# Performance work log

Measured on AMD Instinct MI355X. Metric: run time of the kernel, lower is better.

The kernel has to match this reference:

```python
import jax, jax.numpy as jnp
import numpy as np

N_NODES = 100000
N_EDGES = 1600000
IN_F, HID, N_CLS = 128, 128, 2


def setup_inputs() -> dict:
    key = jax.random.key(0)
    ks = jax.random.split(key, 6)
    return {
        "in_feat": jax.random.normal(ks[0], (N_NODES, IN_F), dtype=jnp.float32),
        "W1": jax.random.normal(ks[1], (IN_F, HID), dtype=jnp.float32) * 0.05,
        "b1": jnp.zeros((HID,), dtype=jnp.float32),
        "W2": jax.random.normal(ks[2], (HID, N_CLS), dtype=jnp.float32) * 0.05,
        "b2": jnp.zeros((N_CLS,), dtype=jnp.float32),
        "src": jax.random.randint(ks[3], (N_EDGES,), 0, N_NODES, dtype=jnp.int32),
        "dst": jax.random.randint(ks[4], (N_EDGES,), 0, N_NODES, dtype=jnp.int32),
    }


def reference(in_feat, W1, b1, W2, b2, src, dst):
    N = in_feat.shape[0]
    ones = jnp.ones(src.shape[0], dtype=in_feat.dtype)
    deg_out = jax.ops.segment_sum(ones, src, num_segments=N)
    deg_in = jax.ops.segment_sum(ones, dst, num_segments=N)
    # DGL norm='both' with allow_zero_in_degree: inf -> 0 for zero-degree nodes
    ninv_out = jnp.where(deg_out > 0, deg_out ** -0.5, 0.0)[:, None]
    ninv_in = jnp.where(deg_in > 0, deg_in ** -0.5, 0.0)[:, None]

    def gconv(x, W, b):
        h = x * ninv_out
        if W.shape[0] > W.shape[1]:
            # mult W first (DGL optimization when in_feats > out_feats)
            h = h @ W
            h = jax.ops.segment_sum(h[src], dst, num_segments=N)
        else:
            h = jax.ops.segment_sum(h[src], dst, num_segments=N)
            h = h @ W
        return h * ninv_in + b

    h = jax.nn.relu(gconv(in_feat, W1, b1))
    return gconv(h, W2, b2)
```

## Files before the change

kernel.cpp:

```cpp
#include <hip/hip_runtime.h>

#define IN_F 128
#define HID  128
#define NB_SHIFT 8
#define NBKT 512
#define NCHUNK 256

typedef __bf16 bf16x8 __attribute__((ext_vector_type(8)));
typedef float f32x4 __attribute__((ext_vector_type(4)));
union U8 { uint4 u; bf16x8 v; };

__device__ __forceinline__ unsigned int bfround(float x) {
    unsigned int u = __float_as_uint(x);
    return (u + 0x7fffu + ((u >> 16) & 1u)) >> 16;
}
__device__ __forceinline__ unsigned int pack2(float a, float b) {
    return bfround(a) | (bfround(b) << 16);
}
__device__ __forceinline__ float lo_f(unsigned int u) { return __uint_as_float(u << 16); }
__device__ __forceinline__ float hi_f(unsigned int u) { return __uint_as_float(u & 0xffff0000u); }

__global__ __launch_bounds__(256)
void countAB_kernel(const int* __restrict__ src, const int* __restrict__ dst,
                    int* __restrict__ cd, int* __restrict__ cs, int E, int epc) {
    __shared__ int hd[NBKT], hs[NBKT];
    int tid = threadIdx.x, c = blockIdx.x;
    hd[tid] = 0; hd[tid + 256] = 0; hs[tid] = 0; hs[tid + 256] = 0;
    __syncthreads();
    int lo = c * epc, hi = min(lo + epc, E);
    for (int i = lo + tid; i < hi; i += 256) {
        atomicAdd(&hd[dst[i] >> NB_SHIFT], 1);
        atomicAdd(&hs[src[i] >> NB_SHIFT], 1);
    }
    __syncthreads();
    cd[c * NBKT + tid] = hd[tid]; cd[c * NBKT + tid + 256] = hd[tid + 256];
    cs[c * NBKT + tid] = hs[tid]; cs[c * NBKT + tid + 256] = hs[tid + 256];
}

__global__ __launch_bounds__(256)
void scanB1_kernel(int* __restrict__ cd, int* __restrict__ cs,
                   int* __restrict__ btd, int* __restrict__ bts) {
    __shared__ int sd[256];
    int b = blockIdx.x, tid = threadIdx.x;
    int* arr = (b < NBKT) ? cd : cs;
    int* bt  = (b < NBKT) ? btd : bts;
    int col = b & (NBKT - 1);
    int v = arr[tid * NBKT + col];
    sd[tid] = v; __syncthreads();
    for (int off = 1; off < 256; off <<= 1) {
        int t = (tid >= off) ? sd[tid - off] : 0;
        __syncthreads();
        sd[tid] += t;
        __syncthreads();
    }
    arr[tid * NBKT + col] = sd[tid] - v;
    if (tid == 255) bt[col] = sd[255];
}

__global__ __launch_bounds__(512)
void scanB2_kernel(const int* __restrict__ btd, const int* __restrict__ bts,
                   int* __restrict__ bbd, int* __restrict__ bbs,
                   int* __restrict__ row_ptr, int N, int E) {
    __shared__ int sd[512];
    int tid = threadIdx.x;
    const int* bt = blockIdx.x ? bts : btd;
    int* bb = blockIdx.x ? bbs : bbd;
    int v = bt[tid];
    sd[tid] = v; __syncthreads();
    for (int off = 1; off < 512; off <<= 1) {
        int t = (tid >= off) ? sd[tid - off] : 0;
        __syncthreads();
        sd[tid] += t;
        __syncthreads();
    }
    bb[tid] = sd[tid] - v;
    if (tid == 511) bb[512] = sd[511];
    if (blockIdx.x == 0 && tid == 0) row_ptr[N] = E;
}

__global__ __launch_bounds__(256)
void scatterAB_kernel(const int* __restrict__ src, const int* __restrict__ dst,
                      const int* __restrict__ cd, const int* __restrict__ cs,
                      const int* __restrict__ bbd, const int* __restrict__ bbs,
                      int* __restrict__ pairs, unsigned char* __restrict__ sbytes,
                      int E, int epc) {
    __shared__ int curd[NBKT], curs[NBKT];
    int tid = threadIdx.x, c = blockIdx.x;
    curd[tid]       = cd[c * NBKT + tid]       + bbd[tid];
    curd[tid + 256] = cd[c * NBKT + tid + 256] + bbd[tid + 256];
    curs[tid]       = cs[c * NBKT + tid]       + bbs[tid];
    curs[tid + 256] = cs[c * NBKT + tid + 256] + bbs[tid + 256];
    __syncthreads();
    int lo = c * epc, hi = min(lo + epc, E);
    for (int i = lo + tid; i < hi; i += 256) {
        int s = src[i], d = dst[i];
        int pd = atomicAdd(&curd[d >> NB_SHIFT], 1);
        pairs[pd] = s | ((d & 255) << 17);
        int ps = atomicAdd(&curs[s >> NB_SHIFT], 1);
        sbytes[ps] = (unsigned char)(s & 255);
    }
}

__global__ __launch_bounds__(256)
void buildD_kernel(const int* __restrict__ pairs, const int* __restrict__ bbd,
                   int* __restrict__ row_ptr, float* __restrict__ ninv_in,
                   int* __restrict__ eidx, int N) {
    __shared__ int cnt[256], sd[256], cursor[256];
    int b = blockIdx.x, tid = threadIdx.x;
    int beg = bbd[b], end = bbd[b + 1];
    cnt[tid] = 0;
    __syncthreads();
    for (int i = beg + tid; i < end; i += 256)
        atomicAdd(&cnt[(pairs[i] >> 17) & 255], 1);
    __syncthreads();
    int v = cnt[tid];
    sd[tid] = v; __syncthreads();
    for (int off = 1; off < 256; off <<= 1) {
        int t = (tid >= off) ? sd[tid - off] : 0;
        __syncthreads();
        sd[tid] += t;
        __syncthreads();
    }
    int excl = sd[tid] - v;
    int node = (b << NB_SHIFT) + tid;
    if (node < N) {
        row_ptr[node] = beg + excl;
        ninv_in[node] = (v > 0) ? rsqrtf((float)v) : 0.0f;
    }
    cursor[tid] = beg + excl;
    __syncthreads();
    for (int i = beg + tid; i < end; i += 256) {
        int p = pairs[i];
        int pos = atomicAdd(&cursor[(p >> 17) & 255], 1);
        eidx[pos] = p & 0x1FFFF;
    }
}

__global__ __launch_bounds__(256)
void buildDsrc_kernel(const unsigned char* __restrict__ sbytes, const int* __restrict__ bbs,
                      float* __restrict__ ninv_out, int N) {
    __shared__ int cnt[256];
    int b = blockIdx.x, tid = threadIdx.x;
    int beg = bbs[b], end = bbs[b + 1];
    cnt[tid] = 0;
    __syncthreads();
    for (int i = beg + tid; i < end; i += 256)
        atomicAdd(&cnt[sbytes[i]], 1);
    __syncthreads();
    int node = (b << NB_SHIFT) + tid;
    if (node < N) {
        int v = cnt[tid];
        ninv_out[node] = (v > 0) ? rsqrtf((float)v) : 0.0f;
    }
}

__global__ __launch_bounds__(256)
void conv_kernel(const float* __restrict__ in_feat, const float* __restrict__ ninv_out,
                 unsigned int* __restrict__ xb, int N) {
    int gid = blockIdx.x * 256 + threadIdx.x;
    if (gid >= N * 32) return;
    int r = gid >> 5, q = gid & 31;
    float no = ninv_out[r];
    float4 v = ((const float4*)in_feat)[(long)r * 32 + q];
    uint2 o;
    o.x = pack2(v.x * no, v.y * no);
    o.y = pack2(v.z * no, v.w * no);
    ((uint2*)xb)[(long)r * 32 + q] = o;
}

__global__ __launch_bounds__(256)
void agg1_kernel(const unsigned int* __restrict__ xb, const int* __restrict__ row_ptr,
                 const int* __restrict__ eidx, unsigned int* __restrict__ Bb, int N) {
    int wave = threadIdx.x >> 6;
    int lane = threadIdx.x & 63;
    int d = blockIdx.x * 4 + wave;
    if (d >= N) return;
    int beg = row_ptr[d], end = row_ptr[d + 1];
    float ax = 0.f, ay = 0.f;
    int j = beg;
    for (; j + 8 <= end; j += 8) {
        int s0 = eidx[j+0], s1 = eidx[j+1], s2 = eidx[j+2], s3 = eidx[j+3];
        int s4 = eidx[j+4], s5 = eidx[j+5], s6 = eidx[j+6], s7 = eidx[j+7];
        unsigned int u0 = xb[(long)s0*64+lane], u1 = xb[(long)s1*64+lane];
        unsigned int u2 = xb[(long)s2*64+lane], u3 = xb[(long)s3*64+lane];
        unsigned int u4 = xb[(long)s4*64+lane], u5 = xb[(long)s5*64+lane];
        unsigned int u6 = xb[(long)s6*64+lane], u7 = xb[(long)s7*64+lane];
        ax += lo_f(u0) + lo_f(u1) + lo_f(u2) + lo_f(u3)
            + lo_f(u4) + lo_f(u5) + lo_f(u6) + lo_f(u7);
        ay += hi_f(u0) + hi_f(u1) + hi_f(u2) + hi_f(u3)
            + hi_f(u4) + hi_f(u5) + hi_f(u6) + hi_f(u7);
    }
    for (; j + 2 <= end; j += 2) {
        unsigned int u0 = xb[(long)eidx[j]*64+lane], u1 = xb[(long)eidx[j+1]*64+lane];
        ax += lo_f(u0) + lo_f(u1);
        ay += hi_f(u0) + hi_f(u1);
    }
    if (j < end) {
        unsigned int u = xb[(long)eidx[j]*64+lane];
        ax += lo_f(u); ay += hi_f(u);
    }
    Bb[(long)d * 64 + lane] = pack2(ax, ay);
}

#define MM_ROWS 64
__global__ __launch_bounds__(256)
void mm1_kernel(const unsigned int* __restrict__ Bb, const float* __restrict__ W1,
                const float* __restrict__ b1, const float* __restrict__ ninv_in,
                const float* __restrict__ ninv_out, const float* __restrict__ W2,
                float* __restrict__ t, int N) {
    __shared__ unsigned int w1t[128 * 68];
    int tid = threadIdx.x;
    int wave = tid >> 6, lane = tid & 63;
    int row0 = blockIdx.x * MM_ROWS;

    {
        int c = tid & 127;
        int kh = tid >> 7;
#pragma unroll 8
        for (int j = 0; j < 32; ++j) {
            int k2 = j * 2 + kh;
            float a = W1[(k2 * 2)     * HID + c];
            float b = W1[(k2 * 2 + 1) * HID + c];
            w1t[c * 68 + k2] = pack2(a, b);
        }
    }

    int m = lane & 15;
    int kg = lane >> 4;
    float  b1r[8];
    float2 w2r[8];
    const float2* W2v = (const float2*)W2;
#pragma unroll
    for (int ct = 0; ct < 8; ++ct) {
        int n = m + 16 * ct;
        b1r[ct] = b1[n];
        w2r[ct] = W2v[n];
    }

    int r = row0 + wave * 16 + m;
    U8 afrag[4];
    if (r < N) {
#pragma unroll
        for (int ks = 0; ks < 4; ++ks)
            afrag[ks].u = *(const uint4*)&Bb[(long)r * 64 + ks * 16 + kg * 4];
    } else {
#pragma unroll
        for (int ks = 0; ks < 4; ++ks)
            afrag[ks].u = make_uint4(0u, 0u, 0u, 0u);
    }
    __syncthreads();

    f32x4 acc[8];
#pragma unroll
    for (int ct = 0; ct < 8; ++ct) acc[ct] = (f32x4){0.f, 0.f, 0.f, 0.f};

#pragma unroll
    for (int ks = 0; ks < 4; ++ks) {
#pragma unroll
        for (int ct = 0; ct < 8; ++ct) {
            U8 bf;
            bf.u = *(const uint4*)&w1t[(m + 16 * ct) * 68 + ks * 16 + kg * 4];
            acc[ct] = __builtin_amdgcn_mfma_f32_16x16x32_bf16(afrag[ks].v, bf.v, acc[ct], 0, 0, 0);
        }
    }

#pragma unroll
    for (int reg = 0; reg < 4; ++reg) {
        int grow = row0 + wave * 16 + kg * 4 + reg;
        int cg = min(grow, N - 1);
        float ni = ninv_in[cg];
        float p0 = 0.f, p1 = 0.f;
#pragma unroll
        for (int ct = 0; ct < 8; ++ct) {
            float h = fmaxf(acc[ct][reg] * ni + b1r[ct], 0.f);
            p0 += h * w2r[ct].x;
            p1 += h * w2r[ct].y;
        }
#pragma unroll
        for (int off = 8; off >= 1; off >>= 1) {
            p0 += __shfl_xor(p0, off, 16);
            p1 += __shfl_xor(p1, off, 16);
        }
        if (m == 0 && grow < N) {
            float no = ninv_out[grow];
            ((float2*)t)[grow] = make_float2(p0 * no, p1 * no);
        }
    }
}

__global__ void final2_kernel(const float* __restrict__ t, const int* __restrict__ row_ptr,
                              const int* __restrict__ eidx, const float* __restrict__ ninv_in,
                              const float* __restrict__ b2, float* __restrict__ out, int N) {
    int i = blockIdx.x * blockDim.x + threadIdx.x;
    if (i >= N) return;
    int beg = row_ptr[i], end = row_ptr[i + 1];
    const float2* t2 = (const float2*)t;
    float ax = 0.f, ay = 0.f;
    int j = beg;
    for (; j + 4 <= end; j += 4) {
        float2 v0 = t2[eidx[j]], v1 = t2[eidx[j+1]], v2 = t2[eidx[j+2]], v3 = t2[eidx[j+3]];
        ax += v0.x + v1.x + v2.x + v3.x;
        ay += v0.y + v1.y + v2.y + v3.y;
    }
    for (; j < end; ++j) {
        float2 v = t2[eidx[j]];
        ax += v.x; ay += v.y;
    }
    float ni = ninv_in[i];
    float2 o;
    o.x = ax * ni + b2[0];
    o.y = ay * ni + b2[1];
    ((float2*)out)[i] = o;
}

extern "C" void kernel_launch(void* const* d_in, const int* in_sizes, int n_in,
                              void* d_out, int out_size, void* d_ws, size_t ws_size,
                              hipStream_t stream) {
    const float* in_feat = (const float*)d_in[0];
    const float* W1      = (const float*)d_in[1];
    const float* b1      = (const float*)d_in[2];
    const float* W2      = (const float*)d_in[3];
    const float* b2      = (const float*)d_in[4];
    const int*   src     = (const int*)d_in[5];
    const int*   dst     = (const int*)d_in[6];
    int N = in_sizes[0] / IN_F;
    int E = in_sizes[5];
    int NB = (N + 255) >> 8;

    unsigned int* Bb  = (unsigned int*)d_ws;
    int*   pairs      = (int*)Bb;
    unsigned char* sbytes = (unsigned char*)(Bb + E);
    unsigned int* xb  = Bb + (size_t)64 * N;
    float* ninv_out   = (float*)(xb + (size_t)64 * N);
    float* ninv_in    = ninv_out + N;
    float* t          = ninv_in + N;
    int*   row_ptr    = (int*)(t + (size_t)2 * N);
    int*   eidx       = row_ptr + N + 1;
    int*   cd         = eidx + E;
    int*   cs         = cd + NCHUNK * NBKT;
    int*   btd        = cs + NCHUNK * NBKT;
    int*   bts        = btd + NBKT;
    int*   bbd        = bts + NBKT;
    int*   bbs        = bbd + NBKT + 1;

    int epc = (E + NCHUNK - 1) / NCHUNK;

    countAB_kernel<<<NCHUNK, 256, 0, stream>>>(src, dst, cd, cs, E, epc);
    scanB1_kernel<<<2 * NBKT, 256, 0, stream>>>(cd, cs, btd, bts);
    scanB2_kernel<<<2, 512, 0, stream>>>(btd, bts, bbd, bbs, row_ptr, N, E);
    scatterAB_kernel<<<NCHUNK, 256, 0, stream>>>(src, dst, cd, cs, bbd, bbs,
                                                 pairs, sbytes, E, epc);
    buildD_kernel<<<NB, 256, 0, stream>>>(pairs, bbd, row_ptr, ninv_in, eidx, N);
    buildDsrc_kernel<<<NB, 256, 0, stream>>>(sbytes, bbs, ninv_out, N);

    conv_kernel<<<(N * 32 + 255) / 256, 256, 0, stream>>>(in_feat, ninv_out, xb, N);

    agg1_kernel<<<(N + 3) / 4, 256, 0, stream>>>(xb, row_ptr, eidx, Bb, N);

    mm1_kernel<<<(N + MM_ROWS - 1) / MM_ROWS, 256, 0, stream>>>(
        Bb, W1, b1, ninv_in, ninv_out, W2, t, N);

    final2_kernel<<<(N + 255) / 256, 256, 0, stream>>>(
        t, row_ptr, eidx, ninv_in, b2, (float*)d_out, N);
}
```

Measured before the change: 258.6 us.

## Merge degree kernels, pretranspose W1 once, widen agg1 gathers to 8-byte loads

Folds the source-degree normalization kernel into the destination CSR build kernel as extra blocks, removing one launch. Packs W1 into bf16 pairs once, using extra blocks of the scan kernel, so each mm1 block loads the packed tile with vector copies instead of strided fp32 loads. agg1 now gives each half-wave a different edge and has lanes fetch uint2 (four bf16 values), combining the halves with a cross-half shuffle. This issues fewer, wider gather loads, at the cost of idle half-waves on nodes with odd degree and a shuffle reduction.

Result: no change. 257.2 us (-0.5%).

```diff
diff --git a/kernel.cpp b/kernel.cpp
--- a/kernel.cpp
+++ b/kernel.cpp
@@ -60,9 +60,18 @@
 __global__ __launch_bounds__(512)
 void scanB2_kernel(const int* __restrict__ btd, const int* __restrict__ bts,
                    int* __restrict__ bbd, int* __restrict__ bbs,
-                   int* __restrict__ row_ptr, int N, int E) {
+                   int* __restrict__ row_ptr, const float* __restrict__ W1,
+                   unsigned int* __restrict__ w1tb, int N, int E) {
+    int tid = threadIdx.x;
+    if (blockIdx.x >= 2) {
+        int idx = (blockIdx.x - 2) * 512 + tid;
+        int c = idx & 127, k2 = idx >> 7;
+        float a = W1[(2 * k2)     * HID + c];
+        float b = W1[(2 * k2 + 1) * HID + c];
+        w1tb[c * 64 + k2] = pack2(a, b);
+        return;
+    }
     __shared__ int sd[512];
-    int tid = threadIdx.x;
     const int* bt = blockIdx.x ? bts : btd;
     int* bb = blockIdx.x ? bbs : bbd;
     int v = bt[tid];
@@ -102,11 +111,29 @@
 }
 
 __global__ __launch_bounds__(256)
-void buildD_kernel(const int* __restrict__ pairs, const int* __restrict__ bbd,
-                   int* __restrict__ row_ptr, float* __restrict__ ninv_in,
-                   int* __restrict__ eidx, int N) {
+void buildD2_kernel(const int* __restrict__ pairs, const unsigned char* __restrict__ sbytes,
+                    const int* __restrict__ bbd, const int* __restrict__ bbs,
+                    int* __restrict__ row_ptr, float* __restrict__ ninv_in,
+                    float* __restrict__ ninv_out, int* __restrict__ eidx,
+                    int N, int NB) {
     __shared__ int cnt[256], sd[256], cursor[256];
-    int b = blockIdx.x, tid = threadIdx.x;
+    int tid = threadIdx.x;
+    if (blockIdx.x >= NB) {
+        int b = blockIdx.x - NB;
+        int beg = bbs[b], end = bbs[b + 1];
+        cnt[tid] = 0;
+        __syncthreads();
+        for (int i = beg + tid; i < end; i += 256)
+            atomicAdd(&cnt[sbytes[i]], 1);
+        __syncthreads();
+        int node = (b << NB_SHIFT) + tid;
+        if (node < N) {
+            int v = cnt[tid];
+            ninv_out[node] = (v > 0) ? rsqrtf((float)v) : 0.0f;
+        }
+        return;
+    }
+    int b = blockIdx.x;
     int beg = bbd[b], end = bbd[b + 1];
     cnt[tid] = 0;
     __syncthreads();
@@ -133,24 +160,6 @@
         int p = pairs[i];
         int pos = atomicAdd(&cursor[(p >> 17) & 255], 1);
         eidx[pos] = p & 0x1FFFF;
-    }
-}
-
-__global__ __launch_bounds__(256)
-void buildDsrc_kernel(const unsigned char* __restrict__ sbytes, const int* __restrict__ bbs,
-                      float* __restrict__ ninv_out, int N) {
-    __shared__ int cnt[256];
-    int b = blockIdx.x, tid = threadIdx.x;
-    int beg = bbs[b], end = bbs[b + 1];
-    cnt[tid] = 0;
-    __syncthreads();
-    for (int i = beg + tid; i < end; i += 256)
-        atomicAdd(&cnt[sbytes[i]], 1);
-    __syncthreads();
-    int node = (b << NB_SHIFT) + tid;
-    if (node < N) {
-        int v = cnt[tid];
-        ninv_out[node] = (v > 0) ? rsqrtf((float)v) : 0.0f;
     }
 }
 
@@ -173,38 +182,55 @@
                  const int* __restrict__ eidx, unsigned int* __restrict__ Bb, int N) {
     int wave = threadIdx.x >> 6;
     int lane = threadIdx.x & 63;
+    int half = lane >> 5;
+    int hl   = lane & 31;
     int d = blockIdx.x * 4 + wave;
     if (d >= N) return;
     int beg = row_ptr[d], end = row_ptr[d + 1];
-    float ax = 0.f, ay = 0.f;
+    const uint2* x2 = (const uint2*)xb;
+    float ax = 0.f, ay = 0.f, az = 0.f, aw = 0.f;
     int j = beg;
-    for (; j + 8 <= end; j += 8) {
-        int s0 = eidx[j+0], s1 = eidx[j+1], s2 = eidx[j+2], s3 = eidx[j+3];
-        int s4 = eidx[j+4], s5 = eidx[j+5], s6 = eidx[j+6], s7 = eidx[j+7];
-        unsigned int u0 = xb[(long)s0*64+lane], u1 = xb[(long)s1*64+lane];
-        unsigned int u2 = xb[(long)s2*64+lane], u3 = xb[(long)s3*64+lane];
-        unsigned int u4 = xb[(long)s4*64+lane], u5 = xb[(long)s5*64+lane];
-        unsigned int u6 = xb[(long)s6*64+lane], u7 = xb[(long)s7*64+lane];
-        ax += lo_f(u0) + lo_f(u1) + lo_f(u2) + lo_f(u3)
-            + lo_f(u4) + lo_f(u5) + lo_f(u6) + lo_f(u7);
-        ay += hi_f(u0) + hi_f(u1) + hi_f(u2) + hi_f(u3)
-            + hi_f(u4) + hi_f(u5) + hi_f(u6) + hi_f(u7);
+    for (; j + 16 <= end; j += 16) {
+        int e0 = eidx[j +  0 + half], e1 = eidx[j +  2 + half];
+        int e2 = eidx[j +  4 + half], e3 = eidx[j +  6 + half];
+        int e4 = eidx[j +  8 + half], e5 = eidx[j + 10 + half];
+        int e6 = eidx[j + 12 + half], e7 = eidx[j + 14 + half];
+        uint2 u0 = x2[(long)e0*32 + hl], u1 = x2[(long)e1*32 + hl];
+        uint2 u2 = x2[(long)e2*32 + hl], u3 = x2[(long)e3*32 + hl];
+        uint2 u4 = x2[(long)e4*32 + hl], u5 = x2[(long)e5*32 + hl];
+        uint2 u6 = x2[(long)e6*32 + hl], u7 = x2[(long)e7*32 + hl];
+        ax += lo_f(u0.x) + lo_f(u1.x) + lo_f(u2.x) + lo_f(u3.x)
+            + lo_f(u4.x) + lo_f(u5.x) + lo_f(u6.x) + lo_f(u7.x);
+        ay += hi_f(u0.x) + hi_f(u1.x) + hi_f(u2.x) + hi_f(u3.x)
+            + hi_f(u4.x) + hi_f(u5.x) + hi_f(u6.x) + hi_f(u7.x);
+        az += lo_f(u0.y) + lo_f(u1.y) + lo_f(u2.y) + lo_f(u3.y)
+            + lo_f(u4.y) + lo_f(u5.y) + lo_f(u6.y) + lo_f(u7.y);
+        aw += hi_f(u0.y) + hi_f(u1.y) + hi_f(u2.y) + hi_f(u3.y)
+            + hi_f(u4.y) + hi_f(u5.y) + hi_f(u6.y) + hi_f(u7.y);
     }
     for (; j + 2 <= end; j += 2) {
-        unsigned int u0 = xb[(long)eidx[j]*64+lane], u1 = xb[(long)eidx[j+1]*64+lane];
-        ax += lo_f(u0) + lo_f(u1);
-        ay += hi_f(u0) + hi_f(u1);
-    }
-    if (j < end) {
-        unsigned int u = xb[(long)eidx[j]*64+lane];
-        ax += lo_f(u); ay += hi_f(u);
-    }
-    Bb[(long)d * 64 + lane] = pack2(ax, ay);
+        int e = eidx[j + half];
+        uint2 u = x2[(long)e*32 + hl];
+        ax += lo_f(u.x); ay += hi_f(u.x); az += lo_f(u.y); aw += hi_f(u.y);
+    }
+    if (j < end && half == 0) {
+        int e = eidx[j];
+        uint2 u = x2[(long)e*32 + hl];
+        ax += lo_f(u.x); ay += hi_f(u.x); az += lo_f(u.y); aw += hi_f(u.y);
+    }
+    ax += __shfl_xor(ax, 32); ay += __shfl_xor(ay, 32);
+    az += __shfl_xor(az, 32); aw += __shfl_xor(aw, 32);
+    if (half == 0) {
+        uint2 o;
+        o.x = pack2(ax, ay);
+        o.y = pack2(az, aw);
+        ((uint2*)Bb)[(long)d * 32 + hl] = o;
+    }
 }
 
 #define MM_ROWS 64
 __global__ __launch_bounds__(256)
-void mm1_kernel(const unsigned int* __restrict__ Bb, const float* __restrict__ W1,
+void mm1_kernel(const unsigned int* __restrict__ Bb, const unsigned int* __restrict__ w1tb,
                 const float* __restrict__ b1, const float* __restrict__ ninv_in,
                 const float* __restrict__ ninv_out, const float* __restrict__ W2,
                 float* __restrict__ t, int N) {
@@ -214,14 +240,12 @@
     int row0 = blockIdx.x * MM_ROWS;
 
     {
-        int c = tid & 127;
-        int kh = tid >> 7;
-#pragma unroll 8
-        for (int j = 0; j < 32; ++j) {
-            int k2 = j * 2 + kh;
-            float a = W1[(k2 * 2)     * HID + c];
-            float b = W1[(k2 * 2 + 1) * HID + c];
-            w1t[c * 68 + k2] = pack2(a, b);
+        const uint4* g = (const uint4*)w1tb;
+#pragma unroll
+        for (int pass = 0; pass < 8; ++pass) {
+            int idx = pass * 256 + tid;
+            int c = idx >> 4, q = idx & 15;
+            *(uint4*)&w1t[c * 68 + q * 4] = g[idx];
         }
     }
 
@@ -342,23 +366,24 @@
     int*   bts        = btd + NBKT;
     int*   bbd        = bts + NBKT;
     int*   bbs        = bbd + NBKT + 1;
+    unsigned int* w1tb = (unsigned int*)(bbs + NBKT + 1);
 
     int epc = (E + NCHUNK - 1) / NCHUNK;
 
     countAB_kernel<<<NCHUNK, 256, 0, stream>>>(src, dst, cd, cs, E, epc);
     scanB1_kernel<<<2 * NBKT, 256, 0, stream>>>(cd, cs, btd, bts);
-    scanB2_kernel<<<2, 512, 0, stream>>>(btd, bts, bbd, bbs, row_ptr, N, E);
+    scanB2_kernel<<<18, 512, 0, stream>>>(btd, bts, bbd, bbs, row_ptr, W1, w1tb, N, E);
     scatterAB_kernel<<<NCHUNK, 256, 0, stream>>>(src, dst, cd, cs, bbd, bbs,
                                                  pairs, sbytes, E, epc);
-    buildD_kernel<<<NB, 256, 0, stream>>>(pairs, bbd, row_ptr, ninv_in, eidx, N);
-    buildDsrc_kernel<<<NB, 256, 0, stream>>>(sbytes, bbs, ninv_out, N);
+    buildD2_kernel<<<2 * NB, 256, 0, stream>>>(pairs, sbytes, bbd, bbs,
+                                               row_ptr, ninv_in, ninv_out, eidx, N, NB);
 
     conv_kernel<<<(N * 32 + 255) / 256, 256, 0, stream>>>(in_feat, ninv_out, xb, N);
 
     agg1_kernel<<<(N + 3) / 4, 256, 0, stream>>>(xb, row_ptr, eidx, Bb, N);
 
     mm1_kernel<<<(N + MM_ROWS - 1) / MM_ROWS, 256, 0, stream>>>(
-        Bb, W1, b1, ninv_in, ninv_out, W2, t, N);
+        Bb, w1tb, b1, ninv_in, ninv_out, W2, t, N);
 
     final2_kernel<<<(N + 255) / 256, 256, 0, stream>>>(
         t, row_ptr, eidx, ninv_in, b2, (float*)d_out, N);
```
